# Optimization experiments

Measured on AMD Instinct MI355X. Metric: run time of the kernel, lower is better.

Reference implementation:

```python
import jax, jax.numpy as jnp
import numpy as np
from jax import lax

EPS = 1e-5
BETA = 0.2  # commitment loss weight


def _conv(x, w, b, stride=2, pad=1):
    # torch Conv2d(k=4, s=2, p=1), NCHW / OIHW
    y = lax.conv_general_dilated(x, w, (stride, stride), [(pad, pad), (pad, pad)],
                                 dimension_numbers=('NCHW', 'OIHW', 'NCHW'))
    return y + b[None, :, None, None]


def _convT(x, w, b):
    # torch ConvTranspose2d(k=4, s=2, p=1): dilated conv with flipped kernel,
    # effective pad = k - 1 - p = 2. w is torch layout [in, out, kH, kW].
    wt = jnp.flip(w, (2, 3)).transpose(1, 0, 2, 3)  # -> [out, in, kH, kW]
    y = lax.conv_general_dilated(x, wt, (1, 1), [(2, 2), (2, 2)], lhs_dilation=(2, 2),
                                 dimension_numbers=('NCHW', 'OIHW', 'NCHW'))
    return y + b[None, :, None, None]


def _bn(x, g, b):
    # BatchNorm2d in training mode: per-channel batch statistics (biased var)
    m = x.mean((0, 2, 3), keepdims=True)
    v = x.var((0, 2, 3), keepdims=True)
    xn = (x - m) * lax.rsqrt(v + EPS)
    return g[None, :, None, None] * xn + b[None, :, None, None]


def _forward(x, enc_w1, enc_b1, enc_w2, enc_b2, enc_w3, enc_b3,
             enc_g1, enc_be1, enc_g2, enc_be2, enc_g3, enc_be3,
             codebook,
             dec_w1, dec_b1, dec_w2, dec_b2, dec_w3, dec_b3,
             dec_g1, dec_be1, dec_g2, dec_be2, dec_g3, dec_be3):
    # ---- Encoder: [B,1,256,256] -> [B,32,32,32] ----
    h = jax.nn.relu(_bn(_conv(x, enc_w1, enc_b1), enc_g1, enc_be1))
    h = jax.nn.relu(_bn(_conv(h, enc_w2, enc_b2), enc_g2, enc_be2))
    q_in = jax.nn.relu(_bn(_conv(h, enc_w3, enc_b3), enc_g3, enc_be3))

    B, C, H, W = q_in.shape
    # ---- Quantiser: cdist + argmin + codebook gather ----
    z = q_in.transpose(0, 2, 3, 1).reshape(B, H * W, C)  # [B, HW, C]
    # squared euclidean distance (same argmin as torch.cdist)
    d2 = (jnp.sum(z * z, -1, keepdims=True)
          - 2.0 * jnp.einsum('bnc,kc->bnk', z, codebook)
          + jnp.sum(codebook * codebook, -1))  # [B, HW, K]
    idx = jnp.argmin(d2, axis=-1)  # [B, HW] int
    q_out = codebook[idx].reshape(B, H, W, C).transpose(0, 3, 1, 2)  # [B,C,H,W]

    commitment = jnp.mean((lax.stop_gradient(q_out) - q_in) ** 2)
    codebook_l = jnp.mean((q_out - lax.stop_gradient(q_in)) ** 2)
    quant_loss = codebook_l + BETA * commitment
    # straight-through estimator
    q_st = q_in + lax.stop_gradient(q_out - q_in)
    encoding_indices = idx.reshape(-1, H, W)

    # ---- Decoder: [B,32,32,32] -> [B,1,256,256] ----
    d = jax.nn.relu(_bn(_convT(q_st, dec_w1, dec_b1), dec_g1, dec_be1))
    d = jax.nn.relu(_bn(_convT(d, dec_w2, dec_b2), dec_g2, dec_be2))
    out = _bn(_convT(d, dec_w3, dec_b3), dec_g3, dec_be3)

    recon = jnp.mean((x - out) ** 2)
    total_loss = quant_loss + recon
    return out, total_loss, encoding_indices


def setup_inputs() -> dict:
    key = jax.random.key(0)
    ks = jax.random.split(key, 12)
    rn = lambda k, s, sc=0.05: jax.random.normal(k, s, jnp.float32) * sc
    inp = {
        'x': jax.random.normal(ks[0], (64, 1, 256, 256), jnp.float32),
        'enc_w1': rn(ks[1], (16, 1, 4, 4)),  'enc_b1': jnp.zeros((16,), jnp.float32),
        'enc_w2': rn(ks[2], (16, 16, 4, 4)), 'enc_b2': jnp.zeros((16,), jnp.float32),
        'enc_w3': rn(ks[3], (32, 16, 4, 4)), 'enc_b3': jnp.zeros((32,), jnp.float32),
        'enc_g1': jnp.ones((16,), jnp.float32), 'enc_be1': jnp.zeros((16,), jnp.float32),
        'enc_g2': jnp.ones((16,), jnp.float32), 'enc_be2': jnp.zeros((16,), jnp.float32),
        'enc_g3': jnp.ones((32,), jnp.float32), 'enc_be3': jnp.zeros((32,), jnp.float32),
        'codebook': jax.random.normal(ks[4], (512, 32), jnp.float32),  # nn.Embedding ~ N(0,1)
        'dec_w1': rn(ks[5], (32, 16, 4, 4)), 'dec_b1': jnp.zeros((16,), jnp.float32),  # [in,out,kH,kW]
        'dec_w2': rn(ks[6], (16, 16, 4, 4)), 'dec_b2': jnp.zeros((16,), jnp.float32),
        'dec_w3': rn(ks[7], (16, 1, 4, 4)),  'dec_b3': jnp.zeros((1,), jnp.float32),
        'dec_g1': jnp.ones((16,), jnp.float32), 'dec_be1': jnp.zeros((16,), jnp.float32),
        'dec_g2': jnp.ones((16,), jnp.float32), 'dec_be2': jnp.zeros((16,), jnp.float32),
        'dec_g3': jnp.ones((1,), jnp.float32),  'dec_be3': jnp.zeros((1,), jnp.float32),
    }
    return inp


def reference(x, enc_w1, enc_b1, enc_w2, enc_b2, enc_w3, enc_b3,
              enc_g1, enc_be1, enc_g2, enc_be2, enc_g3, enc_be3,
              codebook,
              dec_w1, dec_b1, dec_w2, dec_b2, dec_w3, dec_b3,
              dec_g1, dec_be1, dec_g2, dec_be2, dec_g3, dec_be3):
    return _forward(x, enc_w1, enc_b1, enc_w2, enc_b2, enc_w3, enc_b3,
                    enc_g1, enc_be1, enc_g2, enc_be2, enc_g3, enc_be3,
                    codebook,
                    dec_w1, dec_b1, dec_w2, dec_b2, dec_w3, dec_b3,
                    dec_g1, dec_be1, dec_g2, dec_be2, dec_g3, dec_be3)
```

## Files before the change

kernel.cpp:

```cpp
#include <hip/hip_runtime.h>

#define BLK 256


template<int CO>
__device__ __forceinline__ void block_stats(const float* acc, float* partOut) {
  __shared__ float red[2][CO][4];
  const int lane = threadIdx.x & 63;
  const int wv   = threadIdx.x >> 6;
#pragma unroll
  for (int co = 0; co < CO; ++co) {
    float s = acc[co];
    float q = s * s;
#pragma unroll
    for (int off = 32; off > 0; off >>= 1) {
      s += __shfl_down(s, off, 64);
      q += __shfl_down(q, off, 64);
    }
    if (lane == 0) { red[0][co][wv] = s; red[1][co][wv] = q; }
  }
  __syncthreads();
  if (threadIdx.x < CO) {
    const int co = threadIdx.x;
    float s = red[0][co][0] + red[0][co][1] + red[0][co][2] + red[0][co][3];
    float q = red[1][co][0] + red[1][co][1] + red[1][co][2] + red[1][co][3];
    partOut[co * 2]     = s;
    partOut[co * 2 + 1] = q;
  }
}

template<int CO>
__device__ __forceinline__ void block_statsV(const float* s_, const float* q_,
                                             float* partOut) {
  __shared__ float red[2][CO][4];
  const int lane = threadIdx.x & 63;
  const int wv   = threadIdx.x >> 6;
#pragma unroll
  for (int co = 0; co < CO; ++co) {
    float s = s_[co];
    float q = q_[co];
#pragma unroll
    for (int off = 32; off > 0; off >>= 1) {
      s += __shfl_down(s, off, 64);
      q += __shfl_down(q, off, 64);
    }
    if (lane == 0) { red[0][co][wv] = s; red[1][co][wv] = q; }
  }
  __syncthreads();
  if (threadIdx.x < CO) {
    const int co = threadIdx.x;
    float s = red[0][co][0] + red[0][co][1] + red[0][co][2] + red[0][co][3];
    float q = red[1][co][0] + red[1][co][1] + red[1][co][2] + red[1][co][3];
    partOut[co * 2]     = s;
    partOut[co * 2 + 1] = q;
  }
}

__device__ __forceinline__ void block_stats2(float s, float q, float* partOut) {
  __shared__ float red2[2][4];
  const int lane = threadIdx.x & 63;
  const int wv   = threadIdx.x >> 6;
#pragma unroll
  for (int off = 32; off > 0; off >>= 1) {
    s += __shfl_down(s, off, 64);
    q += __shfl_down(q, off, 64);
  }
  if (lane == 0) { red2[0][wv] = s; red2[1][wv] = q; }
  __syncthreads();
  if (threadIdx.x == 0) {
    partOut[0] = red2[0][0] + red2[0][1] + red2[0][2] + red2[0][3];
    partOut[1] = red2[1][0] + red2[1][1] + red2[1][2] + red2[1][3];
  }
}


__global__ __launch_bounds__(BLK) void twc_k(const float* __restrict__ w,
                                             float* __restrict__ wt,
                                             int CI, int CO) {
  const int total = CI * CO * 16;
  for (int i = threadIdx.x; i < total; i += BLK) {
    const int co = i % CO;
    const int rest = i / CO;
    const int kw = rest & 3, kh = (rest >> 2) & 3, ci = rest >> 4;
    wt[i] = w[(co * CI + ci) * 16 + kh * 4 + kw];
  }
}

__global__ __launch_bounds__(BLK) void twt_k(const float* __restrict__ w,
                                             float* __restrict__ wt,
                                             int CI, int CO) {
  const int total = CI * CO * 16;
  for (int i = threadIdx.x; i < total; i += BLK) {
    const int co = i % CO;
    const int rest = i / CO;
    const int kw = rest & 3, kh = (rest >> 2) & 3, ci = rest >> 4;
    wt[i] = w[(ci * CO + co) * 16 + kh * 4 + kw];
  }
}


template<int CI, int CO, int HIN, int WIN, bool BN_IN>
__global__ __launch_bounds__(BLK) void conv_s(
    const float* __restrict__ in, const float* __restrict__ wt,
    const float* __restrict__ bias,
    const float* __restrict__ scIn, const float* __restrict__ shIn,
    float* __restrict__ out, float* __restrict__ part)
{
  constexpr int HOUT = HIN / 2, WOUT = WIN / 2;
  float sc[CI], sh[CI];
  if constexpr (BN_IN) {
#pragma unroll
    for (int ci = 0; ci < CI; ++ci) { sc[ci] = scIn[ci]; sh[ci] = shIn[ci]; }
  }

  const int idx = blockIdx.x * BLK + threadIdx.x;
  const int ow  = idx % WOUT;
  const int oh  = (idx / WOUT) % HOUT;
  const int b   = idx / (WOUT * HOUT);

  float acc[CO];
#pragma unroll
  for (int co = 0; co < CO; ++co) acc[co] = bias[co];

  const float* inb = in + (size_t)b * CI * HIN * WIN;

#pragma unroll
  for (int kh = 0; kh < 4; ++kh) {
    const int ih = oh * 2 - 1 + kh;
    if ((unsigned)ih < (unsigned)HIN) {
#pragma unroll
      for (int kw = 0; kw < 4; ++kw) {
        const int iw = ow * 2 - 1 + kw;
        if ((unsigned)iw < (unsigned)WIN) {
#pragma unroll 2
          for (int ci = 0; ci < CI; ++ci) {
            float v = inb[(ci * HIN + ih) * WIN + iw];
            if constexpr (BN_IN) v = fmaxf(fmaf(sc[ci], v, sh[ci]), 0.f);
            const float* wrow = wt + ((ci * 4 + kh) * 4 + kw) * CO;
#pragma unroll
            for (int co = 0; co < CO; ++co)
              acc[co] = fmaf(v, wrow[co], acc[co]);
          }
        }
      }
    }
  }

#pragma unroll
  for (int co = 0; co < CO; ++co)
    out[((size_t)(b * CO + co) * HOUT + oh) * WOUT + ow] = acc[co];

  block_stats<CO>(acc, part + (size_t)blockIdx.x * CO * 2);
}


template<int CI, int HIN, bool BN_IN>
__global__ __launch_bounds__(BLK) void convTq_k(
    const float* __restrict__ in, const float* __restrict__ wt,
    const float* __restrict__ bias,
    const float* __restrict__ scIn, const float* __restrict__ shIn,
    float* __restrict__ out, float* __restrict__ part)
{
  constexpr int WIN = HIN, HOUT = 2 * HIN, WOUT = 2 * WIN;
  const int idx = blockIdx.x * BLK + threadIdx.x;
  const int qw = idx % WIN;
  const int qh = (idx / WIN) % HIN;
  const int b  = idx / (WIN * HIN);

  constexpr int KH[2][2] = {{1, 3}, {0, 2}};
  constexpr int PR[2][2] = {{1, 0}, {2, 1}};

  float acc[2][2][16];
#pragma unroll
  for (int co = 0; co < 16; ++co) {
    const float bv = bias[co];
    acc[0][0][co] = bv; acc[0][1][co] = bv;
    acc[1][0][co] = bv; acc[1][1][co] = bv;
  }

  const float* inb = in + (size_t)b * CI * HIN * WIN;

#pragma unroll 2
  for (int ci = 0; ci < CI; ++ci) {
    float sci, shi;
    if constexpr (BN_IN) { sci = scIn[ci]; shi = shIn[ci]; }
    const float* base = inb + ci * HIN * WIN;
    float v[3][3];
#pragma unroll
    for (int pr = 0; pr < 3; ++pr) {
      const int ih = qh - 1 + pr;
      const bool okr = (unsigned)ih < (unsigned)HIN;
#pragma unroll
      for (int pc = 0; pc < 3; ++pc) {
        const int iw = qw - 1 + pc;
        float val = 0.f;
        if (okr && (unsigned)iw < (unsigned)WIN) {
          val = base[ih * WIN + iw];
          if constexpr (BN_IN) val = fmaxf(fmaf(sci, val, shi), 0.f);
        }
        v[pr][pc] = val;
      }
    }
#pragma unroll
    for (int py = 0; py < 2; ++py)
#pragma unroll
      for (int tr = 0; tr < 2; ++tr) {
        const int kh = KH[py][tr], pr_ = PR[py][tr];
#pragma unroll
        for (int px = 0; px < 2; ++px)
#pragma unroll
          for (int tc = 0; tc < 2; ++tc) {
            const int kw = KH[px][tc], pc_ = PR[px][tc];
            const float* wrow = wt + ((ci * 4 + kh) * 4 + kw) * 16;
            const float pv = v[pr_][pc_];
#pragma unroll
            for (int co = 0; co < 16; ++co)
              acc[py][px][co] = fmaf(pv, wrow[co], acc[py][px][co]);
          }
      }
  }

  float* ob = out + (size_t)b * 16 * HOUT * WOUT;
#pragma unroll
  for (int co = 0; co < 16; ++co)
#pragma unroll
    for (int py = 0; py < 2; ++py) {
      float2 o; o.x = acc[py][0][co]; o.y = acc[py][1][co];
      *(float2*)&ob[((size_t)co * HOUT + 2 * qh + py) * WOUT + 2 * qw] = o;
    }

  float s[16], q[16];
#pragma unroll
  for (int co = 0; co < 16; ++co) {
    float a = acc[0][0][co] + acc[0][1][co] + acc[1][0][co] + acc[1][1][co];
    float qq = acc[0][0][co] * acc[0][0][co];
    qq = fmaf(acc[0][1][co], acc[0][1][co], qq);
    qq = fmaf(acc[1][0][co], acc[1][0][co], qq);
    qq = fmaf(acc[1][1][co], acc[1][1][co], qq);
    s[co] = a; q[co] = qq;
  }
  block_statsV<16>(s, q, part + (size_t)blockIdx.x * 32);
}


__global__ __launch_bounds__(BLK) void convT3q_k(
    const float* __restrict__ in, const float* __restrict__ w,
    const float* __restrict__ bias,
    const float* __restrict__ scIn, const float* __restrict__ shIn,
    float* __restrict__ out, float* __restrict__ part)
{
  __shared__ float wl[256];
  wl[threadIdx.x] = w[threadIdx.x];
  float sc[16], sh[16];
#pragma unroll
  for (int ci = 0; ci < 16; ++ci) { sc[ci] = scIn[ci]; sh[ci] = shIn[ci]; }
  const float b0 = bias[0];
  __syncthreads();

  const int idx = blockIdx.x * BLK + threadIdx.x;
  const int tx = idx & 63;
  const int ty = (idx >> 6) & 63;
  const int b  = idx >> 12;
  const int i0 = ty * 2, j0 = tx * 2;

  constexpr int TAP[4][4] = {{1,1,3,0},{0,2,2,1},{1,2,3,1},{0,3,2,2}};

  float acc[4][4];
#pragma unroll
  for (int r = 0; r < 4; ++r)
#pragma unroll
    for (int c = 0; c < 4; ++c) acc[r][c] = b0;

  const float* inb = in + (size_t)b * 16 * 16384;

#pragma unroll 4
  for (int ci = 0; ci < 16; ++ci) {
    const float sci = sc[ci], shi = sh[ci];
    const float* base = inb + ci * 16384;
    float v[4][4];
#pragma unroll
    for (int pr = 0; pr < 4; ++pr) {
      const int ih = i0 - 1 + pr;
      const bool okr = (unsigned)ih < 128u;
#pragma unroll
      for (int pc = 0; pc < 4; ++pc) {
        const int iw = j0 - 1 + pc;
        float val = 0.f;
        if (okr && (unsigned)iw < 128u)
          val = fmaxf(fmaf(sci, base[ih * 128 + iw], shi), 0.f);
        v[pr][pc] = val;
      }
    }
    const float4 w0 = *(const float4*)&wl[ci * 16 + 0];
    const float4 w1 = *(const float4*)&wl[ci * 16 + 4];
    const float4 w2 = *(const float4*)&wl[ci * 16 + 8];
    const float4 w3 = *(const float4*)&wl[ci * 16 + 12];
    const float wg[16] = {w0.x,w0.y,w0.z,w0.w, w1.x,w1.y,w1.z,w1.w,
                          w2.x,w2.y,w2.z,w2.w, w3.x,w3.y,w3.z,w3.w};
#pragma unroll
    for (int r = 0; r < 4; ++r) {
      const int k1r = TAP[r][0], p1r = TAP[r][1], k2r = TAP[r][2], p2r = TAP[r][3];
#pragma unroll
      for (int c = 0; c < 4; ++c) {
        const int k1c = TAP[c][0], p1c = TAP[c][1], k2c = TAP[c][2], p2c = TAP[c][3];
        float a = acc[r][c];
        a = fmaf(v[p1r][p1c], wg[k1r * 4 + k1c], a);
        a = fmaf(v[p1r][p2c], wg[k1r * 4 + k2c], a);
        a = fmaf(v[p2r][p1c], wg[k2r * 4 + k1c], a);
        a = fmaf(v[p2r][p2c], wg[k2r * 4 + k2c], a);
        acc[r][c] = a;
      }
    }
  }

  float* ob = out + (size_t)b * 65536;
#pragma unroll
  for (int r = 0; r < 4; ++r) {
    float4 o;
    o.x = acc[r][0]; o.y = acc[r][1]; o.z = acc[r][2]; o.w = acc[r][3];
    *(float4*)&ob[(ty * 4 + r) * 256 + tx * 4] = o;
  }

  float s = 0.f, q = 0.f;
#pragma unroll
  for (int r = 0; r < 4; ++r)
#pragma unroll
    for (int c = 0; c < 4; ++c) { s += acc[r][c]; q = fmaf(acc[r][c], acc[r][c], q); }
  block_stats2(s, q, part + (size_t)blockIdx.x * 2);
}


template<int C>
__global__ __launch_bounds__(BLK) void stats_k(
    const float* __restrict__ part, int nB, double N,
    const float* __restrict__ g, const float* __restrict__ be,
    float* __restrict__ sc, float* __restrict__ sh)
{
  const int c = blockIdx.x;
  double s0 = 0.0, s1 = 0.0;
  for (int i = threadIdx.x; i < nB; i += BLK) {
    s0 += (double)part[(size_t)i * C * 2 + c * 2];
    s1 += (double)part[(size_t)i * C * 2 + c * 2 + 1];
  }
  __shared__ double lds[8];
  const int lane = threadIdx.x & 63, wv = threadIdx.x >> 6;
#pragma unroll
  for (int off = 32; off > 0; off >>= 1) {
    s0 += __shfl_down(s0, off, 64);
    s1 += __shfl_down(s1, off, 64);
  }
  if (lane == 0) { lds[wv * 2] = s0; lds[wv * 2 + 1] = s1; }
  __syncthreads();
  if (threadIdx.x == 0) {
    s0 = lds[0] + lds[2] + lds[4] + lds[6];
    s1 = lds[1] + lds[3] + lds[5] + lds[7];
    const double mean = s0 / N;
    const double var  = s1 / N - mean * mean;
    const double inv  = 1.0 / sqrt(var + 1e-5);
    sc[c] = (float)((double)g[c] * inv);
    sh[c] = (float)((double)be[c] - mean * (double)g[c] * inv);
  }
}


__global__ __launch_bounds__(BLK) void cbn_k(const float* __restrict__ cbg,
                                             float* __restrict__ cbn)
{
  const int k = blockIdx.x * BLK + threadIdx.x;
  float s = 0.f;
#pragma unroll
  for (int c = 0; c < 32; ++c) {
    const float x = cbg[k * 32 + c];
    s = fmaf(x, x, s);
  }
  cbn[k] = s;
}

__global__ __launch_bounds__(BLK) void quantp_k(
    const float* __restrict__ y3, const float* __restrict__ cbg,
    const float* __restrict__ cbnG,
    const float* __restrict__ sc, const float* __restrict__ sh,
    float* __restrict__ bd, int* __restrict__ bki)
{
  __shared__ float cb[64 * 32];
  __shared__ float cbnl[64];
  const int pblk  = blockIdx.x & 63;
  const int chunk = blockIdx.x >> 6;
  for (int i = threadIdx.x; i < 2048; i += BLK) cb[i] = cbg[chunk * 2048 + i];
  if (threadIdx.x < 64) cbnl[threadIdx.x] = cbnG[chunk * 64 + threadIdx.x];
  __syncthreads();

  const int pos0 = pblk * 1024 + threadIdx.x;

  float z[4][32];
#pragma unroll
  for (int c = 0; c < 32; ++c) {
    const float s_ = sc[c], h_ = sh[c];
#pragma unroll
    for (int j = 0; j < 4; ++j) {
      const int pos = pos0 + j * 256;
      const int bb = pos >> 10, pp = pos & 1023;
      z[j][c] = fmaxf(fmaf(s_, y3[((size_t)(bb * 32 + c)) * 1024 + pp], h_), 0.f);
    }
  }

  float best[4] = {3.402823466e38f, 3.402823466e38f, 3.402823466e38f, 3.402823466e38f};
  int   bk[4]   = {0, 0, 0, 0};

  for (int k = 0; k < 64; ++k) {
    const float4* row = (const float4*)&cb[k * 32];
    float d[4] = {0.f, 0.f, 0.f, 0.f};
#pragma unroll
    for (int c4 = 0; c4 < 8; ++c4) {
      const float4 cc = row[c4];
#pragma unroll
      for (int j = 0; j < 4; ++j) {
        d[j] = fmaf(z[j][c4 * 4 + 0], cc.x, d[j]);
        d[j] = fmaf(z[j][c4 * 4 + 1], cc.y, d[j]);
        d[j] = fmaf(z[j][c4 * 4 + 2], cc.z, d[j]);
        d[j] = fmaf(z[j][c4 * 4 + 3], cc.w, d[j]);
      }
    }
    const float cl = cbnl[k];
    const int kk = chunk * 64 + k;
#pragma unroll
    for (int j = 0; j < 4; ++j) {
      const float dd = cl - 2.f * d[j];
      if (dd < best[j]) { best[j] = dd; bk[j] = kk; }
    }
  }

#pragma unroll
  for (int j = 0; j < 4; ++j) {
    const int pos = pos0 + j * 256;
    bd[chunk * 65536 + pos]  = best[j];
    bki[chunk * 65536 + pos] = bk[j];
  }
}

__global__ __launch_bounds__(BLK) void quantm_k(
    const float* __restrict__ y3, const float* __restrict__ cbg,
    const float* __restrict__ sc, const float* __restrict__ sh,
    const float* __restrict__ bd, const int* __restrict__ bki,
    float* __restrict__ qout, float* __restrict__ idx_out,
    float* __restrict__ pq)
{
  const int pos = blockIdx.x * BLK + threadIdx.x;
  float best = 3.402823466e38f;
  int bk = 0;
#pragma unroll
  for (int s = 0; s < 8; ++s) {
    const float d = bd[s * 65536 + pos];
    const int   k = bki[s * 65536 + pos];
    if (d < best) { best = d; bk = k; }
  }

  const int b = pos >> 10, p = pos & 1023;
  const float4* qrow = (const float4*)(cbg + (size_t)bk * 32);
  float msd = 0.f;
#pragma unroll
  for (int c4 = 0; c4 < 8; ++c4) {
    const float4 q4 = qrow[c4];
    const float qv[4] = {q4.x, q4.y, q4.z, q4.w};
#pragma unroll
    for (int u = 0; u < 4; ++u) {
      const int c = c4 * 4 + u;
      const float v  = y3[((size_t)(b * 32 + c)) * 1024 + p];
      const float zz = fmaxf(fmaf(sc[c], v, sh[c]), 0.f);
      const float qq = qv[u];
      qout[((size_t)(b * 32 + c)) * 1024 + p] = zz + (qq - zz);
      const float df = qq - zz;
      msd = fmaf(df, df, msd);
    }
  }
  idx_out[pos] = (float)bk;
  block_stats2(msd, 0.f, pq + (size_t)blockIdx.x * 2);
}


__global__ __launch_bounds__(BLK) void final4_k(
    const float* __restrict__ y6, const float* __restrict__ x,
    const float* __restrict__ sc, const float* __restrict__ sh,
    float* __restrict__ out, float* __restrict__ pr)
{
  const size_t i = ((size_t)blockIdx.x * BLK + threadIdx.x) * 4;
  const float s0 = sc[0], h0 = sh[0];
  const float4 yv = *(const float4*)(y6 + i);
  const float4 xv = *(const float4*)(x + i);
  float4 ov;
  ov.x = fmaf(s0, yv.x, h0);
  ov.y = fmaf(s0, yv.y, h0);
  ov.z = fmaf(s0, yv.z, h0);
  ov.w = fmaf(s0, yv.w, h0);
  *(float4*)(out + i) = ov;
  const float d0 = xv.x - ov.x, d1 = xv.y - ov.y, d2 = xv.z - ov.z, d3 = xv.w - ov.w;
  float s = d0 * d0;
  s = fmaf(d1, d1, s);
  s = fmaf(d2, d2, s);
  s = fmaf(d3, d3, s);
  block_stats2(s, 0.f, pr + (size_t)blockIdx.x * 2);
}


__global__ __launch_bounds__(BLK) void loss_k(
    const float* __restrict__ pq, const float* __restrict__ pr,
    float* __restrict__ lossOut)
{
  double s = 0.0, r = 0.0;
  for (int i = threadIdx.x; i < 256; i += BLK)  s += (double)pq[i * 2];
  for (int i = threadIdx.x; i < 4096; i += BLK) r += (double)pr[i * 2];
  __shared__ double lds[8];
  const int lane = threadIdx.x & 63, wv = threadIdx.x >> 6;
#pragma unroll
  for (int off = 32; off > 0; off >>= 1) {
    s += __shfl_down(s, off, 64);
    r += __shfl_down(r, off, 64);
  }
  if (lane == 0) { lds[wv * 2] = s; lds[wv * 2 + 1] = r; }
  __syncthreads();
  if (threadIdx.x == 0) {
    s = lds[0] + lds[2] + lds[4] + lds[6];
    r = lds[1] + lds[3] + lds[5] + lds[7];
    lossOut[0] = (float)(1.2 * (s / 2097152.0) + r / 4194304.0);
  }
}


extern "C" void kernel_launch(void* const* d_in, const int* in_sizes, int n_in,
                              void* d_out, int out_size, void* d_ws, size_t ws_size,
                              hipStream_t stream) {
  const float* x    = (const float*)d_in[0];
  const float* ew1  = (const float*)d_in[1];
  const float* eb1  = (const float*)d_in[2];
  const float* ew2  = (const float*)d_in[3];
  const float* eb2  = (const float*)d_in[4];
  const float* ew3  = (const float*)d_in[5];
  const float* eb3  = (const float*)d_in[6];
  const float* eg1  = (const float*)d_in[7];
  const float* ebe1 = (const float*)d_in[8];
  const float* eg2  = (const float*)d_in[9];
  const float* ebe2 = (const float*)d_in[10];
  const float* eg3  = (const float*)d_in[11];
  const float* ebe3 = (const float*)d_in[12];
  const float* cbk  = (const float*)d_in[13];
  const float* dw1  = (const float*)d_in[14];
  const float* db1  = (const float*)d_in[15];
  const float* dw2  = (const float*)d_in[16];
  const float* db2  = (const float*)d_in[17];
  const float* dw3  = (const float*)d_in[18];
  const float* db3  = (const float*)d_in[19];
  const float* dg1  = (const float*)d_in[20];
  const float* dbe1 = (const float*)d_in[21];
  const float* dg2  = (const float*)d_in[22];
  const float* dbe2 = (const float*)d_in[23];
  const float* dg3  = (const float*)d_in[24];
  const float* dbe3 = (const float*)d_in[25];

  float* ws = (float*)d_ws;
  float* outp = (float*)d_out;

  float* SC = ws;
  float* SH = ws + 192;
  float* P1 = ws + 1024;
  float* P2 = ws + 132096;
  float* P3 = ws + 164864;
  float* P4 = ws + 181248;
  float* P5 = ws + 214016;
  float* P6 = ws + 345088;
  float* Pq = ws + 377856;
  float* Pr = ws + 378368;
  float* CBN = ws + 411648;
  float* WT1  = ws + 412160;
  float* WT2  = WT1 + 256;
  float* WT3  = WT2 + 4096;
  float* WTD1 = WT3 + 8192;
  float* WTD2 = WTD1 + 8192;

  float* y1 = ws + 524288;
  float* y2 = y1 + 16777216;
  float* y3 = y2 + 4194304;
  float* qo = y3 + 2097152;
  float* y6 = qo + 2097152;
  float* y4 = y2;
  float* y5 = y1;
  float* bd  = y2;
  int*   bki = (int*)(y2 + 524288);

  float* sc1 = SC + 0,  *sh1 = SH + 0;
  float* sc2 = SC + 32, *sh2 = SH + 32;
  float* sc3 = SC + 64, *sh3 = SH + 64;
  float* sc4 = SC + 96, *sh4 = SH + 96;
  float* sc5 = SC + 128,*sh5 = SH + 128;
  float* sc6 = SC + 160,*sh6 = SH + 160;

  twc_k<<<1, BLK, 0, stream>>>(ew1, WT1, 1, 16);
  twc_k<<<1, BLK, 0, stream>>>(ew2, WT2, 16, 16);
  twc_k<<<1, BLK, 0, stream>>>(ew3, WT3, 16, 32);
  twt_k<<<1, BLK, 0, stream>>>(dw1, WTD1, 32, 16);
  twt_k<<<1, BLK, 0, stream>>>(dw2, WTD2, 16, 16);
  cbn_k<<<2, BLK, 0, stream>>>(cbk, CBN);

  conv_s<1, 16, 256, 256, false><<<4096, BLK, 0, stream>>>(x,  WT1, eb1, nullptr, nullptr, y1, P1);
  stats_k<16><<<16, BLK, 0, stream>>>(P1, 4096, 1048576.0, eg1, ebe1, sc1, sh1);
  conv_s<16, 16, 128, 128, true><<<1024, BLK, 0, stream>>>(y1, WT2, eb2, sc1, sh1, y2, P2);
  stats_k<16><<<16, BLK, 0, stream>>>(P2, 1024, 262144.0, eg2, ebe2, sc2, sh2);
  conv_s<16, 32, 64, 64, true><<<256, BLK, 0, stream>>>(y2, WT3, eb3, sc2, sh2, y3, P3);
  stats_k<32><<<32, BLK, 0, stream>>>(P3, 256, 65536.0, eg3, ebe3, sc3, sh3);

  quantp_k<<<512, BLK, 0, stream>>>(y3, cbk, CBN, sc3, sh3, bd, bki);
  quantm_k<<<256, BLK, 0, stream>>>(y3, cbk, sc3, sh3, bd, bki, qo, outp + 4194305, Pq);

  convTq_k<32, 32, false><<<256, BLK, 0, stream>>>(qo, WTD1, db1, nullptr, nullptr, y4, P4);
  stats_k<16><<<16, BLK, 0, stream>>>(P4, 256, 262144.0, dg1, dbe1, sc4, sh4);
  convTq_k<16, 64, true><<<1024, BLK, 0, stream>>>(y4, WTD2, db2, sc4, sh4, y5, P5);
  stats_k<16><<<16, BLK, 0, stream>>>(P5, 1024, 1048576.0, dg2, dbe2, sc5, sh5);
  convT3q_k<<<1024, BLK, 0, stream>>>(y5, dw3, db3, sc5, sh5, y6, P6);
  stats_k<1><<<1, BLK, 0, stream>>>(P6, 1024, 4194304.0, dg3, dbe3, sc6, sh6);

  final4_k<<<4096, BLK, 0, stream>>>(y6, x, sc6, sh6, outp, Pr);
  loss_k<<<1, BLK, 0, stream>>>(Pq, Pr, outp + 4194304);
}
```

Measured before the change: 672.6 us.

## Split output channels across wavefronts in conv and transposed-conv kernels

Encoder convs and the first two decoder transposed convs now give each wavefront a subset of output channels (CGN groups) over a tile of positions, so each thread keeps fewer accumulators. Block sizes, grid sizes and the per-block statistics reduction change to match, with a per-wave shuffle reduction followed by a shared-memory combine. The aim is lower register pressure and higher occupancy or more parallelism on the small decoder grids. The cost is that input values are loaded redundantly by each channel group.

Result: slower. 940.4 us (+39.8%).

```diff
diff --git a/kernel.cpp b/kernel.cpp
--- a/kernel.cpp
+++ b/kernel.cpp
@@ -2,59 +2,6 @@
 
 #define BLK 256
 
-
-template<int CO>
-__device__ __forceinline__ void block_stats(const float* acc, float* partOut) {
-  __shared__ float red[2][CO][4];
-  const int lane = threadIdx.x & 63;
-  const int wv   = threadIdx.x >> 6;
-#pragma unroll
-  for (int co = 0; co < CO; ++co) {
-    float s = acc[co];
-    float q = s * s;
-#pragma unroll
-    for (int off = 32; off > 0; off >>= 1) {
-      s += __shfl_down(s, off, 64);
-      q += __shfl_down(q, off, 64);
-    }
-    if (lane == 0) { red[0][co][wv] = s; red[1][co][wv] = q; }
-  }
-  __syncthreads();
-  if (threadIdx.x < CO) {
-    const int co = threadIdx.x;
-    float s = red[0][co][0] + red[0][co][1] + red[0][co][2] + red[0][co][3];
-    float q = red[1][co][0] + red[1][co][1] + red[1][co][2] + red[1][co][3];
-    partOut[co * 2]     = s;
-    partOut[co * 2 + 1] = q;
-  }
-}
-
-template<int CO>
-__device__ __forceinline__ void block_statsV(const float* s_, const float* q_,
-                                             float* partOut) {
-  __shared__ float red[2][CO][4];
-  const int lane = threadIdx.x & 63;
-  const int wv   = threadIdx.x >> 6;
-#pragma unroll
-  for (int co = 0; co < CO; ++co) {
-    float s = s_[co];
-    float q = q_[co];
-#pragma unroll
-    for (int off = 32; off > 0; off >>= 1) {
-      s += __shfl_down(s, off, 64);
-      q += __shfl_down(q, off, 64);
-    }
-    if (lane == 0) { red[0][co][wv] = s; red[1][co][wv] = q; }
-  }
-  __syncthreads();
-  if (threadIdx.x < CO) {
-    const int co = threadIdx.x;
-    float s = red[0][co][0] + red[0][co][1] + red[0][co][2] + red[0][co][3];
-    float q = red[1][co][0] + red[1][co][1] + red[1][co][2] + red[1][co][3];
-    partOut[co * 2]     = s;
-    partOut[co * 2 + 1] = q;
-  }
-}
 
 __device__ __forceinline__ void block_stats2(float s, float q, float* partOut) {
   __shared__ float red2[2][4];
@@ -99,28 +46,35 @@
 }
 
 
-template<int CI, int CO, int HIN, int WIN, bool BN_IN>
-__global__ __launch_bounds__(BLK) void conv_s(
+template<int CI, int CO, int CGN, int PW, int HIN, int WIN, bool BN_IN>
+__global__ __launch_bounds__(64 * PW * CGN) void conv_cg(
     const float* __restrict__ in, const float* __restrict__ wt,
     const float* __restrict__ bias,
     const float* __restrict__ scIn, const float* __restrict__ shIn,
     float* __restrict__ out, float* __restrict__ part)
 {
   constexpr int HOUT = HIN / 2, WOUT = WIN / 2;
+  constexpr int COG = CO / CGN;
+  const int lane = threadIdx.x & 63;
+  const int w    = threadIdx.x >> 6;
+  const int pw   = w & (PW - 1);
+  const int cg   = w / PW;
+  const int co0  = cg * COG;
+
   float sc[CI], sh[CI];
   if constexpr (BN_IN) {
 #pragma unroll
     for (int ci = 0; ci < CI; ++ci) { sc[ci] = scIn[ci]; sh[ci] = shIn[ci]; }
   }
 
-  const int idx = blockIdx.x * BLK + threadIdx.x;
-  const int ow  = idx % WOUT;
-  const int oh  = (idx / WOUT) % HOUT;
-  const int b   = idx / (WOUT * HOUT);
-
-  float acc[CO];
-#pragma unroll
-  for (int co = 0; co < CO; ++co) acc[co] = bias[co];
+  const int pos = blockIdx.x * (64 * PW) + pw * 64 + lane;
+  const int ow  = pos % WOUT;
+  const int oh  = (pos / WOUT) % HOUT;
+  const int b   = pos / (WOUT * HOUT);
+
+  float acc[COG];
+#pragma unroll
+  for (int j = 0; j < COG; ++j) acc[j] = bias[co0 + j];
 
   const float* inb = in + (size_t)b * CI * HIN * WIN;
 
@@ -136,10 +90,10 @@
           for (int ci = 0; ci < CI; ++ci) {
             float v = inb[(ci * HIN + ih) * WIN + iw];
             if constexpr (BN_IN) v = fmaxf(fmaf(sc[ci], v, sh[ci]), 0.f);
-            const float* wrow = wt + ((ci * 4 + kh) * 4 + kw) * CO;
-#pragma unroll
-            for (int co = 0; co < CO; ++co)
-              acc[co] = fmaf(v, wrow[co], acc[co]);
+            const float* wrow = wt + ((ci * 4 + kh) * 4 + kw) * CO + co0;
+#pragma unroll
+            for (int j = 0; j < COG; ++j)
+              acc[j] = fmaf(v, wrow[j], acc[j]);
           }
         }
       }
@@ -147,35 +101,69 @@
   }
 
 #pragma unroll
-  for (int co = 0; co < CO; ++co)
-    out[((size_t)(b * CO + co) * HOUT + oh) * WOUT + ow] = acc[co];
-
-  block_stats<CO>(acc, part + (size_t)blockIdx.x * CO * 2);
-}
-
-
-template<int CI, int HIN, bool BN_IN>
-__global__ __launch_bounds__(BLK) void convTq_k(
+  for (int j = 0; j < COG; ++j)
+    out[((size_t)(b * CO + co0 + j) * HOUT + oh) * WOUT + ow] = acc[j];
+
+  float s[COG], q[COG];
+#pragma unroll
+  for (int j = 0; j < COG; ++j) { s[j] = acc[j]; q[j] = acc[j] * acc[j]; }
+#pragma unroll
+  for (int off = 32; off > 0; off >>= 1)
+#pragma unroll
+    for (int j = 0; j < COG; ++j) {
+      s[j] += __shfl_down(s[j], off, 64);
+      q[j] += __shfl_down(q[j], off, 64);
+    }
+  __shared__ float red[CGN * PW][COG][2];
+  if (lane == 0) {
+#pragma unroll
+    for (int j = 0; j < COG; ++j) { red[w][j][0] = s[j]; red[w][j][1] = q[j]; }
+  }
+  __syncthreads();
+  if (threadIdx.x < CO) {
+    const int co = threadIdx.x;
+    const int cg2 = co / COG, j = co % COG;
+    float ss = 0.f, qq = 0.f;
+#pragma unroll
+    for (int p2 = 0; p2 < PW; ++p2) {
+      ss += red[cg2 * PW + p2][j][0];
+      qq += red[cg2 * PW + p2][j][1];
+    }
+    part[(size_t)blockIdx.x * CO * 2 + co * 2]     = ss;
+    part[(size_t)blockIdx.x * CO * 2 + co * 2 + 1] = qq;
+  }
+}
+
+
+template<int CI, int CGN, int PW, int HIN, bool BN_IN>
+__global__ __launch_bounds__(64 * PW * CGN) void convTq_cg(
     const float* __restrict__ in, const float* __restrict__ wt,
     const float* __restrict__ bias,
     const float* __restrict__ scIn, const float* __restrict__ shIn,
     float* __restrict__ out, float* __restrict__ part)
 {
   constexpr int WIN = HIN, HOUT = 2 * HIN, WOUT = 2 * WIN;
-  const int idx = blockIdx.x * BLK + threadIdx.x;
-  const int qw = idx % WIN;
-  const int qh = (idx / WIN) % HIN;
-  const int b  = idx / (WIN * HIN);
+  constexpr int COG = 16 / CGN;
+  const int lane = threadIdx.x & 63;
+  const int w    = threadIdx.x >> 6;
+  const int pw   = w & (PW - 1);
+  const int cg   = w / PW;
+  const int co0  = cg * COG;
+
+  const int q_  = blockIdx.x * (64 * PW) + pw * 64 + lane;
+  const int qw  = q_ % WIN;
+  const int qh  = (q_ / WIN) % HIN;
+  const int b   = q_ / (WIN * HIN);
 
   constexpr int KH[2][2] = {{1, 3}, {0, 2}};
   constexpr int PR[2][2] = {{1, 0}, {2, 1}};
 
-  float acc[2][2][16];
-#pragma unroll
-  for (int co = 0; co < 16; ++co) {
-    const float bv = bias[co];
-    acc[0][0][co] = bv; acc[0][1][co] = bv;
-    acc[1][0][co] = bv; acc[1][1][co] = bv;
+  float acc[2][2][COG];
+#pragma unroll
+  for (int j = 0; j < COG; ++j) {
+    const float bv = bias[co0 + j];
+    acc[0][0][j] = bv; acc[0][1][j] = bv;
+    acc[1][0][j] = bv; acc[1][1][j] = bv;
   }
 
   const float* inb = in + (size_t)b * CI * HIN * WIN;
@@ -211,35 +199,59 @@
 #pragma unroll
           for (int tc = 0; tc < 2; ++tc) {
             const int kw = KH[px][tc], pc_ = PR[px][tc];
-            const float* wrow = wt + ((ci * 4 + kh) * 4 + kw) * 16;
+            const float* wrow = wt + ((ci * 4 + kh) * 4 + kw) * 16 + co0;
             const float pv = v[pr_][pc_];
 #pragma unroll
-            for (int co = 0; co < 16; ++co)
-              acc[py][px][co] = fmaf(pv, wrow[co], acc[py][px][co]);
+            for (int j = 0; j < COG; ++j)
+              acc[py][px][j] = fmaf(pv, wrow[j], acc[py][px][j]);
           }
       }
   }
 
   float* ob = out + (size_t)b * 16 * HOUT * WOUT;
 #pragma unroll
-  for (int co = 0; co < 16; ++co)
+  for (int j = 0; j < COG; ++j)
 #pragma unroll
     for (int py = 0; py < 2; ++py) {
-      float2 o; o.x = acc[py][0][co]; o.y = acc[py][1][co];
-      *(float2*)&ob[((size_t)co * HOUT + 2 * qh + py) * WOUT + 2 * qw] = o;
-    }
-
-  float s[16], q[16];
-#pragma unroll
-  for (int co = 0; co < 16; ++co) {
-    float a = acc[0][0][co] + acc[0][1][co] + acc[1][0][co] + acc[1][1][co];
-    float qq = acc[0][0][co] * acc[0][0][co];
-    qq = fmaf(acc[0][1][co], acc[0][1][co], qq);
-    qq = fmaf(acc[1][0][co], acc[1][0][co], qq);
-    qq = fmaf(acc[1][1][co], acc[1][1][co], qq);
-    s[co] = a; q[co] = qq;
-  }
-  block_statsV<16>(s, q, part + (size_t)blockIdx.x * 32);
+      float2 o; o.x = acc[py][0][j]; o.y = acc[py][1][j];
+      *(float2*)&ob[((size_t)(co0 + j) * HOUT + 2 * qh + py) * WOUT + 2 * qw] = o;
+    }
+
+  float s[COG], q[COG];
+#pragma unroll
+  for (int j = 0; j < COG; ++j) {
+    float a = acc[0][0][j] + acc[0][1][j] + acc[1][0][j] + acc[1][1][j];
+    float qq = acc[0][0][j] * acc[0][0][j];
+    qq = fmaf(acc[0][1][j], acc[0][1][j], qq);
+    qq = fmaf(acc[1][0][j], acc[1][0][j], qq);
+    qq = fmaf(acc[1][1][j], acc[1][1][j], qq);
+    s[j] = a; q[j] = qq;
+  }
+#pragma unroll
+  for (int off = 32; off > 0; off >>= 1)
+#pragma unroll
+    for (int j = 0; j < COG; ++j) {
+      s[j] += __shfl_down(s[j], off, 64);
+      q[j] += __shfl_down(q[j], off, 64);
+    }
+  __shared__ float red[CGN * PW][COG][2];
+  if (lane == 0) {
+#pragma unroll
+    for (int j = 0; j < COG; ++j) { red[w][j][0] = s[j]; red[w][j][1] = q[j]; }
+  }
+  __syncthreads();
+  if (threadIdx.x < 16) {
+    const int co = threadIdx.x;
+    const int cg2 = co / COG, j = co % COG;
+    float ss = 0.f, qq = 0.f;
+#pragma unroll
+    for (int p2 = 0; p2 < PW; ++p2) {
+      ss += red[cg2 * PW + p2][j][0];
+      qq += red[cg2 * PW + p2][j][1];
+    }
+    part[(size_t)blockIdx.x * 32 + co * 2]     = ss;
+    part[(size_t)blockIdx.x * 32 + co * 2 + 1] = qq;
+  }
 }
 
 
@@ -600,20 +612,20 @@
   twt_k<<<1, BLK, 0, stream>>>(dw2, WTD2, 16, 16);
   cbn_k<<<2, BLK, 0, stream>>>(cbk, CBN);
 
-  conv_s<1, 16, 256, 256, false><<<4096, BLK, 0, stream>>>(x,  WT1, eb1, nullptr, nullptr, y1, P1);
+  conv_cg<1, 16, 2, 4, 256, 256, false><<<4096, 512, 0, stream>>>(x,  WT1, eb1, nullptr, nullptr, y1, P1);
   stats_k<16><<<16, BLK, 0, stream>>>(P1, 4096, 1048576.0, eg1, ebe1, sc1, sh1);
-  conv_s<16, 16, 128, 128, true><<<1024, BLK, 0, stream>>>(y1, WT2, eb2, sc1, sh1, y2, P2);
+  conv_cg<16, 16, 2, 4, 128, 128, true><<<1024, 512, 0, stream>>>(y1, WT2, eb2, sc1, sh1, y2, P2);
   stats_k<16><<<16, BLK, 0, stream>>>(P2, 1024, 262144.0, eg2, ebe2, sc2, sh2);
-  conv_s<16, 32, 64, 64, true><<<256, BLK, 0, stream>>>(y2, WT3, eb3, sc2, sh2, y3, P3);
+  conv_cg<16, 32, 4, 4, 64, 64, true><<<256, 1024, 0, stream>>>(y2, WT3, eb3, sc2, sh2, y3, P3);
   stats_k<32><<<32, BLK, 0, stream>>>(P3, 256, 65536.0, eg3, ebe3, sc3, sh3);
 
   quantp_k<<<512, BLK, 0, stream>>>(y3, cbk, CBN, sc3, sh3, bd, bki);
   quantm_k<<<256, BLK, 0, stream>>>(y3, cbk, sc3, sh3, bd, bki, qo, outp + 4194305, Pq);
 
-  convTq_k<32, 32, false><<<256, BLK, 0, stream>>>(qo, WTD1, db1, nullptr, nullptr, y4, P4);
-  stats_k<16><<<16, BLK, 0, stream>>>(P4, 256, 262144.0, dg1, dbe1, sc4, sh4);
-  convTq_k<16, 64, true><<<1024, BLK, 0, stream>>>(y4, WTD2, db2, sc4, sh4, y5, P5);
-  stats_k<16><<<16, BLK, 0, stream>>>(P5, 1024, 1048576.0, dg2, dbe2, sc5, sh5);
+  convTq_cg<32, 4, 1, 32, false><<<1024, 256, 0, stream>>>(qo, WTD1, db1, nullptr, nullptr, y4, P4);
+  stats_k<16><<<16, BLK, 0, stream>>>(P4, 1024, 262144.0, dg1, dbe1, sc4, sh4);
+  convTq_cg<16, 2, 2, 64, true><<<2048, 256, 0, stream>>>(y4, WTD2, db2, sc4, sh4, y5, P5);
+  stats_k<16><<<16, BLK, 0, stream>>>(P5, 2048, 1048576.0, dg2, dbe2, sc5, sh5);
   convT3q_k<<<1024, BLK, 0, stream>>>(y5, dw3, db3, sc5, sh5, y6, P6);
   stats_k<1><<<1, BLK, 0, stream>>>(P6, 1024, 4194304.0, dg3, dbe3, sc6, sh6);
 
```
